# Optimization experiments

Hardware: AMD Instinct MI355X
Metric: run time of the kernel (lower is better)

The kernel has to match this reference:

```python
import jax, jax.numpy as jnp
import numpy as np

B, N, S, D1, D2 = 16, 4096, 1024, 128, 256
MLP = [256, 128]
BN_EPS = 1e-5


def setup_inputs() -> dict:
    key = jax.random.key(0)
    ks = jax.random.split(key, 12)
    inp = {
        "xyz1": jax.random.normal(ks[0], (B, 3, N), dtype=jnp.float32),
        "xyz2": jax.random.normal(ks[1], (B, 3, S), dtype=jnp.float32),
        "points1": jax.random.normal(ks[2], (B, D1, N), dtype=jnp.float32),
        "points2": jax.random.normal(ks[3], (B, D2, S), dtype=jnp.float32),
    }
    in_ch = D1 + D2  # 384
    chans = [in_ch] + MLP
    ki = 4
    for li in range(len(MLP)):
        cin, cout = chans[li], chans[li + 1]
        inp[f"w{li+1}"] = jax.random.normal(ks[ki], (cout, cin), dtype=jnp.float32) * (1.0 / np.sqrt(cin)); ki += 1
        inp[f"b{li+1}"] = jnp.zeros((cout,), dtype=jnp.float32)
        inp[f"g{li+1}"] = jnp.ones((cout,), dtype=jnp.float32)
        inp[f"beta{li+1}"] = jnp.zeros((cout,), dtype=jnp.float32)
    return inp


def _batchnorm1d(x, gamma, beta):
    # x: [B, C, N]; training-mode batch stats over (B, N)
    mean = jnp.mean(x, axis=(0, 2), keepdims=True)
    var = jnp.var(x, axis=(0, 2), keepdims=True)
    xhat = (x - mean) * jax.lax.rsqrt(var + BN_EPS)
    return xhat * gamma[None, :, None] + beta[None, :, None]


def reference(xyz1, xyz2, points1, points2, w1, b1, g1, beta1, w2, b2, g2, beta2):
    x1 = jnp.transpose(xyz1, (0, 2, 1))   # [B, N, 3]
    x2 = jnp.transpose(xyz2, (0, 2, 1))   # [B, S, 3]
    p2 = jnp.transpose(points2, (0, 2, 1))  # [B, S, D2]

    # squared pairwise distances [B, N, S]
    dists = jnp.sum((x1[:, :, None, :] - x2[:, None, :, :]) ** 2, axis=-1)
    # 3 smallest distances (original sorts then slices top-3)
    neg_d3, idx = jax.lax.top_k(-dists, 3)  # [B, N, 3]
    d3 = -neg_d3
    dist_recip = 1.0 / (d3 + 1e-8)
    weight = dist_recip / jnp.sum(dist_recip, axis=2, keepdims=True)  # [B, N, 3]

    # gather neighbor features: [B, N, 3, D2]
    feats = p2[jnp.arange(p2.shape[0])[:, None, None], idx]
    interp = jnp.sum(feats * weight[..., None], axis=2)  # [B, N, D2]

    p1 = jnp.transpose(points1, (0, 2, 1))  # [B, N, D1]
    new_points = jnp.concatenate([p1, interp], axis=-1)  # [B, N, D1+D2]
    x = jnp.transpose(new_points, (0, 2, 1))  # [B, C, N]

    for w, b, g, bt in ((w1, b1, g1, beta1), (w2, b2, g2, beta2)):
        x = jnp.einsum("oc,bcn->bon", w, x) + b[None, :, None]
        x = _batchnorm1d(x, g, bt)
        x = jax.nn.relu(x)
    return x
```

## Files before the change

kernel.cpp:

```cpp
#include <hip/hip_runtime.h>

typedef unsigned short u16;
typedef unsigned int   u32;
typedef __attribute__((ext_vector_type(8))) short bf16x8;
typedef __attribute__((ext_vector_type(4))) float f32x4;

#define NB   16
#define NPTS 4096
#define SPTS 1024
#define BNT  65536

__device__ __forceinline__ float bf2f(u16 u){ return __uint_as_float(((u32)u)<<16); }
__device__ __forceinline__ u16 f2bf(float f){
  u32 u = __float_as_uint(f);
  return (u16)((u + 0x7FFFu + ((u>>16)&1u))>>16);
}

__global__ __launch_bounds__(256) void convw_k(const float* __restrict__ w1, const float* __restrict__ w2,
                                               u16* __restrict__ w1b, u16* __restrict__ w2b){
  int i = blockIdx.x*256 + threadIdx.x;
  if (i < 98304) w1b[i] = f2bf(w1[i]);
  else { int j = i - 98304; w2b[j] = f2bf(w2[j]); }
}

__global__ __launch_bounds__(256) void transpose_k(const float* __restrict__ in, u16* __restrict__ out,
                                                   int C, int S, int ostride){
  __shared__ float tl[64][65];
  int t = threadIdx.x;
  int b = blockIdx.y;
  int s0 = blockIdx.x * 64;
  for (int ct = 0; ct < C; ct += 64){
    __syncthreads();
    for (int i = t; i < 4096; i += 256){
      int sl = i & 63, cl = i >> 6;
      tl[sl][cl] = in[((size_t)b*C + ct + cl)*S + s0 + sl];
    }
    __syncthreads();
    for (int i = t; i < 4096; i += 256){
      int cl = i & 63, sl = i >> 6;
      out[((size_t)b*S + s0 + sl)*ostride + ct + cl] = f2bf(tl[sl][cl]);
    }
  }
}

__global__ __launch_bounds__(512) void knn_k(const float* __restrict__ xyz1, const float* __restrict__ xyz2,
                                             const u16* __restrict__ p2t, u16* __restrict__ X){
  __shared__ float4 sxyz[SPTS];
  __shared__ float  pd[8][3][64];
  __shared__ int    pi[8][3][64];
  __shared__ float  swts[3][64];
  __shared__ int    sidx[3][64];
  int t  = threadIdx.x;
  int b  = blockIdx.x >> 6;
  int n0 = (blockIdx.x & 63) << 6;
  const float* x2b = xyz2 + (size_t)b*3*SPTS;
  for (int s = t; s < SPTS; s += 512)
    sxyz[s] = make_float4(x2b[s], x2b[SPTS+s], x2b[2*SPTS+s], 0.f);
  int q = t & 63, g = t >> 6;
  const float* x1b = xyz1 + (size_t)b*3*NPTS;
  int n = n0 + q;
  float qx = x1b[n], qy = x1b[NPTS+n], qz = x1b[2*NPTS+n];
  __syncthreads();

  float d0=3.4e38f, d1=3.4e38f, d2=3.4e38f;
  int   i0=0, i1=0, i2=0;
  int sBeg = g << 7, sEnd = sBeg + 128;
  for (int s = sBeg; s < sEnd; ++s){
    float4 p = sxyz[s];
    float dist;
    {
      #pragma clang fp contract(off)
      float dx = qx - p.x, dy = qy - p.y, dz = qz - p.z;
      dist = ((dx*dx) + (dy*dy)) + (dz*dz);
    }
    if (dist < d2){
      bool c1 = dist < d1, c0 = dist < d0;
      d2 = c1 ? d1 : dist;                 i2 = c1 ? i1 : s;
      float nd1 = c1 ? (c0 ? d0 : dist) : d1;
      int   ni1 = c1 ? (c0 ? i0 : s)    : i1;
      d0 = c0 ? dist : d0;                 i0 = c0 ? s : i0;
      d1 = nd1;                            i1 = ni1;
    }
  }
  pd[g][0][q]=d0; pd[g][1][q]=d1; pd[g][2][q]=d2;
  pi[g][0][q]=i0; pi[g][1][q]=i1; pi[g][2][q]=i2;
  __syncthreads();

  if (t < 64){
    float m0=3.4e38f, m1=3.4e38f, m2=3.4e38f;
    int   j0=0, j1=0, j2=0;
    #pragma unroll
    for (int gg = 0; gg < 8; ++gg){
      #pragma unroll
      for (int p = 0; p < 3; ++p){
        float dist = pd[gg][p][t]; int s = pi[gg][p][t];
        if (dist < m2){
          bool c1 = dist < m1, c0 = dist < m0;
          m2 = c1 ? m1 : dist;                 j2 = c1 ? j1 : s;
          float nd1 = c1 ? (c0 ? m0 : dist) : m1;
          int   ni1 = c1 ? (c0 ? j0 : s)    : j1;
          m0 = c0 ? dist : m0;                 j0 = c0 ? s : j0;
          m1 = nd1;                            j1 = ni1;
        }
      }
    }
    float r0 = 1.f/(m0 + 1e-8f), r1 = 1.f/(m1 + 1e-8f), r2 = 1.f/(m2 + 1e-8f);
    float rs = (r0 + r1) + r2;
    swts[0][t] = r0/rs; swts[1][t] = r1/rs; swts[2][t] = r2/rs;
    sidx[0][t] = j0;    sidx[1][t] = j1;    sidx[2][t] = j2;
  }
  __syncthreads();

  int w = t >> 6, lane = t & 63;
  for (int qq = w*8; qq < w*8 + 8; ++qq){
    float wa = swts[0][qq], wb = swts[1][qq], wc = swts[2][qq];
    int   j0 = sidx[0][qq], j1 = sidx[1][qq], j2 = sidx[2][qq];
    const ushort4 u0 = *(const ushort4*)(p2t + (((size_t)b*SPTS + j0)<<8) + (lane<<2));
    const ushort4 u1 = *(const ushort4*)(p2t + (((size_t)b*SPTS + j1)<<8) + (lane<<2));
    const ushort4 u2 = *(const ushort4*)(p2t + (((size_t)b*SPTS + j2)<<8) + (lane<<2));
    ushort4 ov;
    ov.x = f2bf(wa*bf2f(u0.x) + wb*bf2f(u1.x) + wc*bf2f(u2.x));
    ov.y = f2bf(wa*bf2f(u0.y) + wb*bf2f(u1.y) + wc*bf2f(u2.y));
    ov.z = f2bf(wa*bf2f(u0.z) + wb*bf2f(u1.z) + wc*bf2f(u2.z));
    ov.w = f2bf(wa*bf2f(u0.w) + wb*bf2f(u1.w) + wc*bf2f(u2.w));
    *(ushort4*)(X + ((size_t)b*NPTS + n0 + qq)*384 + 128 + (lane<<2)) = ov;
  }
}

__global__ __launch_bounds__(256) void gemm_k(const u16* __restrict__ A, const u16* __restrict__ Bw,
                                              u16* __restrict__ Cc, int K, int Nn,
                                              float* __restrict__ gsum, float* __restrict__ gsq){
  __shared__ u16 lA[128*32];
  __shared__ u16 lB[128*32];
  __shared__ float sums[128];
  __shared__ float sqs[128];
  int t = threadIdx.x, lane = t & 63, wid = t >> 6;
  int rowBase = blockIdx.x << 7, colBase = blockIdx.y << 7;
  int wm = wid >> 1, wn = wid & 1;
  int rr = lane >> 2, cb = (lane & 3) << 4;

  const char* pA0 = (const char*)A  + (((size_t)(rowBase + wid*32 + rr) * K) << 1) + cb;
  const char* pA1 = pA0 + (((size_t)16 * K) << 1);
  const char* pB0 = (const char*)Bw + (((size_t)(colBase + wid*32 + rr) * K) << 1) + cb;
  const char* pB1 = pB0 + (((size_t)16 * K) << 1);
  char* dA0 = (char*)lA + wid*2048; char* dA1 = dA0 + 1024;
  char* dB0 = (char*)lB + wid*2048; char* dB1 = dB0 + 1024;

  f32x4 z = {0.f, 0.f, 0.f, 0.f};
  f32x4 acc[4][4];
  #pragma unroll
  for (int m = 0; m < 4; ++m)
    #pragma unroll
    for (int n = 0; n < 4; ++n) acc[m][n] = z;

  for (int kk = 0; kk < K; kk += 32){
    size_t ko = ((size_t)kk) << 1;
    __builtin_amdgcn_global_load_lds((const __attribute__((address_space(1))) void*)(pA0 + ko),
                                     (__attribute__((address_space(3))) void*)dA0, 16, 0, 0);
    __builtin_amdgcn_global_load_lds((const __attribute__((address_space(1))) void*)(pA1 + ko),
                                     (__attribute__((address_space(3))) void*)dA1, 16, 0, 0);
    __builtin_amdgcn_global_load_lds((const __attribute__((address_space(1))) void*)(pB0 + ko),
                                     (__attribute__((address_space(3))) void*)dB0, 16, 0, 0);
    __builtin_amdgcn_global_load_lds((const __attribute__((address_space(1))) void*)(pB1 + ko),
                                     (__attribute__((address_space(3))) void*)dB1, 16, 0, 0);
    __syncthreads();
    bf16x8 af[4], bfr[4];
    #pragma unroll
    for (int m = 0; m < 4; ++m)
      af[m] = *(const bf16x8*)(lA + ((wm*64 + m*16 + (lane & 15)) << 5) + ((lane >> 4) << 3));
    #pragma unroll
    for (int n = 0; n < 4; ++n)
      bfr[n] = *(const bf16x8*)(lB + ((wn*64 + n*16 + (lane & 15)) << 5) + ((lane >> 4) << 3));
    #pragma unroll
    for (int m = 0; m < 4; ++m)
      #pragma unroll
      for (int n = 0; n < 4; ++n)
        acc[m][n] = __builtin_amdgcn_mfma_f32_16x16x32_bf16(af[m], bfr[n], acc[m][n], 0, 0, 0);
    __syncthreads();
  }

  if (t < 128){ sums[t] = 0.f; sqs[t] = 0.f; }
  __syncthreads();
  size_t rb = (size_t)rowBase + wm*64 + ((lane >> 4) << 2);
  int cbase = colBase + wn*64 + (lane & 15);
  #pragma unroll
  for (int n = 0; n < 4; ++n){
    float s = 0.f, q = 0.f;
    #pragma unroll
    for (int m = 0; m < 4; ++m){
      #pragma unroll
      for (int r = 0; r < 4; ++r){
        float v = acc[m][n][r];
        Cc[(rb + m*16 + r)*(size_t)Nn + cbase + n*16] = f2bf(v);
        s += v; q += v*v;
      }
    }
    int cl = wn*64 + n*16 + (lane & 15);
    atomicAdd(&sums[cl], s); atomicAdd(&sqs[cl], q);
  }
  __syncthreads();
  if (t < 128){
    atomicAdd(&gsum[colBase + t], sums[t]);
    atomicAdd(&gsq [colBase + t], sqs[t]);
  }
}

__global__ void finalize_k(const float* __restrict__ sum, const float* __restrict__ sq,
                           const float* __restrict__ g, const float* __restrict__ bet,
                           float* __restrict__ sc, float* __restrict__ sh, int C){
  int t = threadIdx.x;
  if (t < C){
    const float inv = 1.f/65536.f;
    float mean = sum[t]*inv;
    float var  = sq[t]*inv - mean*mean;
    float rstd = rsqrtf(var + 1e-5f);
    float s = g[t]*rstd;
    sc[t] = s;
    sh[t] = bet[t] - mean*s;
  }
}

__global__ __launch_bounds__(256) void bnrelu_k(const u16* __restrict__ y, u16* __restrict__ o,
                                                const float* __restrict__ sc, const float* __restrict__ sh){
  size_t i = ((size_t)blockIdx.x*256 + threadIdx.x)*8;
  ushort4 a = *(const ushort4*)(y + i);
  ushort4 b = *(const ushort4*)(y + i + 4);
  int c0 = (int)(i & 255);
  ushort4 oa, ob;
  float v;
  v = bf2f(a.x)*sc[c0+0] + sh[c0+0]; oa.x = f2bf(fmaxf(v, 0.f));
  v = bf2f(a.y)*sc[c0+1] + sh[c0+1]; oa.y = f2bf(fmaxf(v, 0.f));
  v = bf2f(a.z)*sc[c0+2] + sh[c0+2]; oa.z = f2bf(fmaxf(v, 0.f));
  v = bf2f(a.w)*sc[c0+3] + sh[c0+3]; oa.w = f2bf(fmaxf(v, 0.f));
  v = bf2f(b.x)*sc[c0+4] + sh[c0+4]; ob.x = f2bf(fmaxf(v, 0.f));
  v = bf2f(b.y)*sc[c0+5] + sh[c0+5]; ob.y = f2bf(fmaxf(v, 0.f));
  v = bf2f(b.z)*sc[c0+6] + sh[c0+6]; ob.z = f2bf(fmaxf(v, 0.f));
  v = bf2f(b.w)*sc[c0+7] + sh[c0+7]; ob.w = f2bf(fmaxf(v, 0.f));
  *(ushort4*)(o + i)     = oa;
  *(ushort4*)(o + i + 4) = ob;
}

__global__ __launch_bounds__(256) void finalout_k(const u16* __restrict__ y2, const float* __restrict__ sc,
                                                  const float* __restrict__ sh, float* __restrict__ out){
  __shared__ float tl[128][65];
  int t  = threadIdx.x;
  int b  = blockIdx.x >> 6;
  int n0 = (blockIdx.x & 63) << 6;
  for (int i = t; i < 8192; i += 256){
    int r = i >> 7, c = i & 127;
    float v = bf2f(y2[((size_t)b*NPTS + n0 + r)*128 + c]);
    v = fmaxf(v*sc[c] + sh[c], 0.f);
    tl[c][r] = v;
  }
  __syncthreads();
  for (int i = t; i < 8192; i += 256){
    int o = i >> 6, j = i & 63;
    out[(size_t)b*128*NPTS + (size_t)o*NPTS + n0 + j] = tl[o][j];
  }
}

extern "C" void kernel_launch(void* const* d_in, const int* in_sizes, int n_in,
                              void* d_out, int out_size, void* d_ws, size_t ws_size,
                              hipStream_t stream) {
  const float* xyz1    = (const float*)d_in[0];
  const float* xyz2    = (const float*)d_in[1];
  const float* points1 = (const float*)d_in[2];
  const float* points2 = (const float*)d_in[3];
  const float* w1      = (const float*)d_in[4];
  const float* g1      = (const float*)d_in[6];
  const float* beta1   = (const float*)d_in[7];
  const float* w2      = (const float*)d_in[8];
  const float* g2      = (const float*)d_in[10];
  const float* beta2   = (const float*)d_in[11];

  char* ws = (char*)d_ws;
  u16*  X    = (u16*)ws;
  u16*  Y1n  = (u16*)ws;
  u16*  Y2   = (u16*)(ws + 33554432);
  u16*  p2t  = (u16*)(ws + 50331648);
  u16*  Y1   = (u16*)(ws + 58720256);
  u16*  w1b  = (u16*)(ws + 92274688);
  u16*  w2b  = (u16*)(ws + 92471296);
  float* st  = (float*)(ws + 92536832);
  float* sum1 = st;        float* sq1 = st + 256;
  float* sum2 = st + 512;  float* sq2 = st + 640;
  float* sc1  = st + 768;  float* sh1 = st + 1024;
  float* sc2  = st + 1280; float* sh2 = st + 1408;

  hipMemsetAsync(st, 0, 768*sizeof(float), stream);

  convw_k<<<512, 256, 0, stream>>>(w1, w2, w1b, w2b);
  transpose_k<<<dim3(64, 16), 256, 0, stream>>>(points1, X,   128, NPTS, 384);
  transpose_k<<<dim3(16, 16), 256, 0, stream>>>(points2, p2t, 256, SPTS, 256);
  knn_k<<<1024, 512, 0, stream>>>(xyz1, xyz2, p2t, X);
  gemm_k<<<dim3(512, 2), 256, 0, stream>>>(X, w1b, Y1, 384, 256, sum1, sq1);
  finalize_k<<<1, 256, 0, stream>>>(sum1, sq1, g1, beta1, sc1, sh1, 256);
  bnrelu_k<<<8192, 256, 0, stream>>>(Y1, Y1n, sc1, sh1);
  gemm_k<<<dim3(512, 1), 256, 0, stream>>>(Y1n, w2b, Y2, 256, 128, sum2, sq2);
  finalize_k<<<1, 256, 0, stream>>>(sum2, sq2, g2, beta2, sc2, sh2, 128);
  finalout_k<<<1024, 256, 0, stream>>>(Y2, sc2, sh2, (float*)d_out);
}
```

Before: 168.1 us.

## Fuse BN1+ReLU into second GEMM, swizzled 64x128 tiles, partial-sum BN stats

Removes the standalone BN+ReLU pass by applying scale/shift/ReLU while staging the second GEMM's A operand into LDS. The two GEMMs are rewritten with 64x128 tiles, K-step 64 and an XOR-swizzled LDS layout to reduce bank conflicts. BN statistics use per-block partial sums reduced by a multi-block finalize kernel instead of global atomics and a memset. The second GEMM's A path now goes through registers rather than direct global-to-LDS loads, which may add latency.

```diff
diff --git a/kernel.cpp b/kernel.cpp
--- a/kernel.cpp
+++ b/kernel.cpp
@@ -3,6 +3,7 @@
 typedef unsigned short u16;
 typedef unsigned int   u32;
 typedef __attribute__((ext_vector_type(8))) short bf16x8;
+typedef __attribute__((ext_vector_type(8))) unsigned short u16x8;
 typedef __attribute__((ext_vector_type(4))) float f32x4;
 
 #define NB   16
@@ -127,117 +128,252 @@
   }
 }
 
-__global__ __launch_bounds__(256) void gemm_k(const u16* __restrict__ A, const u16* __restrict__ Bw,
-                                              u16* __restrict__ Cc, int K, int Nn,
-                                              float* __restrict__ gsum, float* __restrict__ gsq){
-  __shared__ u16 lA[128*32];
-  __shared__ u16 lB[128*32];
-  __shared__ float sums[128];
-  __shared__ float sqs[128];
+
+__global__ __launch_bounds__(256) void gemm1_k(const u16* __restrict__ A, const u16* __restrict__ Bw,
+                                               u16* __restrict__ Cc,
+                                               float* __restrict__ psum, float* __restrict__ psq){
+  const int K = 384, Nn = 256;
+  __shared__ u16 lA[64*64];
+  __shared__ u16 lB[128*64];
+  __shared__ float sums[128], sqs[128];
   int t = threadIdx.x, lane = t & 63, wid = t >> 6;
-  int rowBase = blockIdx.x << 7, colBase = blockIdx.y << 7;
+  int rowBase = blockIdx.x << 6, colBase = blockIdx.y << 7;
   int wm = wid >> 1, wn = wid & 1;
-  int rr = lane >> 2, cb = (lane & 3) << 4;
-
-  const char* pA0 = (const char*)A  + (((size_t)(rowBase + wid*32 + rr) * K) << 1) + cb;
-  const char* pA1 = pA0 + (((size_t)16 * K) << 1);
-  const char* pB0 = (const char*)Bw + (((size_t)(colBase + wid*32 + rr) * K) << 1) + cb;
-  const char* pB1 = pB0 + (((size_t)16 * K) << 1);
-  char* dA0 = (char*)lA + wid*2048; char* dA1 = dA0 + 1024;
-  char* dB0 = (char*)lB + wid*2048; char* dB1 = dB0 + 1024;
-
-  f32x4 z = {0.f, 0.f, 0.f, 0.f};
-  f32x4 acc[4][4];
-  #pragma unroll
-  for (int m = 0; m < 4; ++m)
+
+  const char* pA[2]; char* dA[2];
+  #pragma unroll
+  for (int j = 0; j < 2; ++j){
+    int L = j*4096 + wid*1024 + lane*16;
+    int row = L >> 7, kb = L & 127;
+    int kbs = kb ^ ((row & 7) << 4);
+    pA[j] = (const char*)A + ((size_t)(rowBase + row)*K)*2 + kbs;
+    dA[j] = (char*)lA + j*4096 + wid*1024;
+  }
+  const char* pB[4]; char* dB[4];
+  #pragma unroll
+  for (int j = 0; j < 4; ++j){
+    int L = j*4096 + wid*1024 + lane*16;
+    int row = L >> 7, kb = L & 127;
+    int kbs = kb ^ ((row & 7) << 4);
+    pB[j] = (const char*)Bw + ((size_t)(colBase + row)*K)*2 + kbs;
+    dB[j] = (char*)lB + j*4096 + wid*1024;
+  }
+
+  f32x4 z = {0.f,0.f,0.f,0.f};
+  f32x4 acc[2][4];
+  #pragma unroll
+  for (int m = 0; m < 2; ++m)
     #pragma unroll
     for (int n = 0; n < 4; ++n) acc[m][n] = z;
 
-  for (int kk = 0; kk < K; kk += 32){
-    size_t ko = ((size_t)kk) << 1;
-    __builtin_amdgcn_global_load_lds((const __attribute__((address_space(1))) void*)(pA0 + ko),
-                                     (__attribute__((address_space(3))) void*)dA0, 16, 0, 0);
-    __builtin_amdgcn_global_load_lds((const __attribute__((address_space(1))) void*)(pA1 + ko),
-                                     (__attribute__((address_space(3))) void*)dA1, 16, 0, 0);
-    __builtin_amdgcn_global_load_lds((const __attribute__((address_space(1))) void*)(pB0 + ko),
-                                     (__attribute__((address_space(3))) void*)dB0, 16, 0, 0);
-    __builtin_amdgcn_global_load_lds((const __attribute__((address_space(1))) void*)(pB1 + ko),
-                                     (__attribute__((address_space(3))) void*)dB1, 16, 0, 0);
-    __syncthreads();
-    bf16x8 af[4], bfr[4];
-    #pragma unroll
-    for (int m = 0; m < 4; ++m)
-      af[m] = *(const bf16x8*)(lA + ((wm*64 + m*16 + (lane & 15)) << 5) + ((lane >> 4) << 3));
-    #pragma unroll
-    for (int n = 0; n < 4; ++n)
-      bfr[n] = *(const bf16x8*)(lB + ((wn*64 + n*16 + (lane & 15)) << 5) + ((lane >> 4) << 3));
-    #pragma unroll
-    for (int m = 0; m < 4; ++m)
-      #pragma unroll
-      for (int n = 0; n < 4; ++n)
-        acc[m][n] = __builtin_amdgcn_mfma_f32_16x16x32_bf16(af[m], bfr[n], acc[m][n], 0, 0, 0);
+  for (int kk = 0; kk < K; kk += 64){
+    size_t ko = (size_t)kk * 2;
+    #pragma unroll
+    for (int j = 0; j < 2; ++j)
+      __builtin_amdgcn_global_load_lds((const __attribute__((address_space(1))) void*)(pA[j] + ko),
+                                       (__attribute__((address_space(3))) void*)dA[j], 16, 0, 0);
+    #pragma unroll
+    for (int j = 0; j < 4; ++j)
+      __builtin_amdgcn_global_load_lds((const __attribute__((address_space(1))) void*)(pB[j] + ko),
+                                       (__attribute__((address_space(3))) void*)dB[j], 16, 0, 0);
+    __syncthreads();
+    bf16x8 af[2][2], bfv[4][2];
+    #pragma unroll
+    for (int m = 0; m < 2; ++m){
+      int row = wm*32 + m*16 + (lane & 15);
+      int sw = (row & 7) << 4;
+      #pragma unroll
+      for (int ks = 0; ks < 2; ++ks){
+        int kb = (ks*64 + ((lane >> 4) << 4)) ^ sw;
+        af[m][ks] = *(const bf16x8*)((const char*)lA + row*128 + kb);
+      }
+    }
+    #pragma unroll
+    for (int n = 0; n < 4; ++n){
+      int row = wn*64 + n*16 + (lane & 15);
+      int sw = (row & 7) << 4;
+      #pragma unroll
+      for (int ks = 0; ks < 2; ++ks){
+        int kb = (ks*64 + ((lane >> 4) << 4)) ^ sw;
+        bfv[n][ks] = *(const bf16x8*)((const char*)lB + row*128 + kb);
+      }
+    }
+    #pragma unroll
+    for (int ks = 0; ks < 2; ++ks)
+      #pragma unroll
+      for (int m = 0; m < 2; ++m)
+        #pragma unroll
+        for (int n = 0; n < 4; ++n)
+          acc[m][n] = __builtin_amdgcn_mfma_f32_16x16x32_bf16(af[m][ks], bfv[n][ks], acc[m][n], 0, 0, 0);
     __syncthreads();
   }
 
   if (t < 128){ sums[t] = 0.f; sqs[t] = 0.f; }
   __syncthreads();
-  size_t rb = (size_t)rowBase + wm*64 + ((lane >> 4) << 2);
-  int cbase = colBase + wn*64 + (lane & 15);
+  int colb = colBase + wn*64 + (lane & 15);
+  int rowb = rowBase + wm*32 + ((lane >> 4) << 2);
   #pragma unroll
   for (int n = 0; n < 4; ++n){
-    float s = 0.f, q = 0.f;
-    #pragma unroll
-    for (int m = 0; m < 4; ++m){
+    float s = 0.f, qq2 = 0.f;
+    #pragma unroll
+    for (int m = 0; m < 2; ++m){
       #pragma unroll
       for (int r = 0; r < 4; ++r){
         float v = acc[m][n][r];
-        Cc[(rb + m*16 + r)*(size_t)Nn + cbase + n*16] = f2bf(v);
-        s += v; q += v*v;
-      }
-    }
-    int cl = wn*64 + n*16 + (lane & 15);
-    atomicAdd(&sums[cl], s); atomicAdd(&sqs[cl], q);
+        Cc[(size_t)(rowb + m*16 + r)*Nn + colb + n*16] = f2bf(v);
+        s += v; qq2 += v*v;
+      }
+    }
+    atomicAdd(&sums[wn*64 + n*16 + (lane & 15)], s);
+    atomicAdd(&sqs [wn*64 + n*16 + (lane & 15)], qq2);
   }
   __syncthreads();
   if (t < 128){
-    atomicAdd(&gsum[colBase + t], sums[t]);
-    atomicAdd(&gsq [colBase + t], sqs[t]);
-  }
-}
-
-__global__ void finalize_k(const float* __restrict__ sum, const float* __restrict__ sq,
-                           const float* __restrict__ g, const float* __restrict__ bet,
-                           float* __restrict__ sc, float* __restrict__ sh, int C){
-  int t = threadIdx.x;
-  if (t < C){
+    int c = colBase + t;
+    psum[(size_t)c*1024 + blockIdx.x] = sums[t];
+    psq [(size_t)c*1024 + blockIdx.x] = sqs[t];
+  }
+}
+
+__global__ __launch_bounds__(256) void gemm2_k(const u16* __restrict__ A, const u16* __restrict__ Bw,
+                                               u16* __restrict__ Cc,
+                                               const float* __restrict__ sc, const float* __restrict__ sh,
+                                               float* __restrict__ psum, float* __restrict__ psq){
+  const int K = 256, Nn = 128;
+  __shared__ u16 lA[64*64];
+  __shared__ u16 lB[128*64];
+  __shared__ float sums[128], sqs[128];
+  int t = threadIdx.x, lane = t & 63, wid = t >> 6;
+  int rowBase = blockIdx.x << 6;
+  int wm = wid >> 1, wn = wid & 1;
+
+  const char* pB[4]; char* dB[4];
+  #pragma unroll
+  for (int j = 0; j < 4; ++j){
+    int L = j*4096 + wid*1024 + lane*16;
+    int row = L >> 7, kb = L & 127;
+    int kbs = kb ^ ((row & 7) << 4);
+    pB[j] = (const char*)Bw + ((size_t)row*K)*2 + kbs;
+    dB[j] = (char*)lB + j*4096 + wid*1024;
+  }
+  int arow = t & 63, achunk = t >> 6;
+  const u16* pArow = A + (size_t)(rowBase + arow)*K + achunk*16;
+  int asw = (arow & 7) << 4;
+  char* wA0 = (char*)lA + arow*128 + (((achunk*32)      ) ^ asw);
+  char* wA1 = (char*)lA + arow*128 + (((achunk*32) + 16 ) ^ asw);
+
+  f32x4 z = {0.f,0.f,0.f,0.f};
+  f32x4 acc[2][4];
+  #pragma unroll
+  for (int m = 0; m < 2; ++m)
+    #pragma unroll
+    for (int n = 0; n < 4; ++n) acc[m][n] = z;
+
+  for (int kk = 0; kk < K; kk += 64){
+    size_t ko = (size_t)kk * 2;
+    #pragma unroll
+    for (int j = 0; j < 4; ++j)
+      __builtin_amdgcn_global_load_lds((const __attribute__((address_space(1))) void*)(pB[j] + ko),
+                                       (__attribute__((address_space(3))) void*)dB[j], 16, 0, 0);
+    u16x8 y0 = *(const u16x8*)(pArow + kk);
+    u16x8 y1 = *(const u16x8*)(pArow + kk + 8);
+    int k0 = kk + achunk*16;
+    bf16x8 o0, o1;
+    #pragma unroll
+    for (int j = 0; j < 8; ++j){
+      float v = bf2f((u16)y0[j]) * sc[k0 + j] + sh[k0 + j];
+      o0[j] = (short)f2bf(fmaxf(v, 0.f));
+    }
+    #pragma unroll
+    for (int j = 0; j < 8; ++j){
+      float v = bf2f((u16)y1[j]) * sc[k0 + 8 + j] + sh[k0 + 8 + j];
+      o1[j] = (short)f2bf(fmaxf(v, 0.f));
+    }
+    *(bf16x8*)wA0 = o0;
+    *(bf16x8*)wA1 = o1;
+    __syncthreads();
+    bf16x8 af[2][2], bfv[4][2];
+    #pragma unroll
+    for (int m = 0; m < 2; ++m){
+      int row = wm*32 + m*16 + (lane & 15);
+      int sw = (row & 7) << 4;
+      #pragma unroll
+      for (int ks = 0; ks < 2; ++ks){
+        int kb = (ks*64 + ((lane >> 4) << 4)) ^ sw;
+        af[m][ks] = *(const bf16x8*)((const char*)lA + row*128 + kb);
+      }
+    }
+    #pragma unroll
+    for (int n = 0; n < 4; ++n){
+      int row = wn*64 + n*16 + (lane & 15);
+      int sw = (row & 7) << 4;
+      #pragma unroll
+      for (int ks = 0; ks < 2; ++ks){
+        int kb = (ks*64 + ((lane >> 4) << 4)) ^ sw;
+        bfv[n][ks] = *(const bf16x8*)((const char*)lB + row*128 + kb);
+      }
+    }
+    #pragma unroll
+    for (int ks = 0; ks < 2; ++ks)
+      #pragma unroll
+      for (int m = 0; m < 2; ++m)
+        #pragma unroll
+        for (int n = 0; n < 4; ++n)
+          acc[m][n] = __builtin_amdgcn_mfma_f32_16x16x32_bf16(af[m][ks], bfv[n][ks], acc[m][n], 0, 0, 0);
+    __syncthreads();
+  }
+
+  if (t < 128){ sums[t] = 0.f; sqs[t] = 0.f; }
+  __syncthreads();
+  int colb = wn*64 + (lane & 15);
+  int rowb = rowBase + wm*32 + ((lane >> 4) << 2);
+  #pragma unroll
+  for (int n = 0; n < 4; ++n){
+    float s = 0.f, qq2 = 0.f;
+    #pragma unroll
+    for (int m = 0; m < 2; ++m){
+      #pragma unroll
+      for (int r = 0; r < 4; ++r){
+        float v = acc[m][n][r];
+        Cc[(size_t)(rowb + m*16 + r)*Nn + colb + n*16] = f2bf(v);
+        s += v; qq2 += v*v;
+      }
+    }
+    atomicAdd(&sums[colb + n*16], s);
+    atomicAdd(&sqs [colb + n*16], qq2);
+  }
+  __syncthreads();
+  if (t < 128){
+    psum[(size_t)t*1024 + blockIdx.x] = sums[t];
+    psq [(size_t)t*1024 + blockIdx.x] = sqs[t];
+  }
+}
+
+__global__ __launch_bounds__(256) void finalize2_k(const float* __restrict__ psum, const float* __restrict__ psq,
+                                                   const float* __restrict__ g, const float* __restrict__ bet,
+                                                   float* __restrict__ sc, float* __restrict__ sh){
+  __shared__ float rs[256], rq[256];
+  int c = blockIdx.x, t = threadIdx.x;
+  float s = 0.f, q = 0.f;
+  for (int rt = t; rt < 1024; rt += 256){
+    s += psum[(size_t)c*1024 + rt];
+    q += psq [(size_t)c*1024 + rt];
+  }
+  rs[t] = s; rq[t] = q;
+  __syncthreads();
+  for (int off = 128; off; off >>= 1){
+    if (t < off){ rs[t] += rs[t+off]; rq[t] += rq[t+off]; }
+    __syncthreads();
+  }
+  if (t == 0){
     const float inv = 1.f/65536.f;
-    float mean = sum[t]*inv;
-    float var  = sq[t]*inv - mean*mean;
+    float mean = rs[0]*inv;
+    float var  = rq[0]*inv - mean*mean;
     float rstd = rsqrtf(var + 1e-5f);
-    float s = g[t]*rstd;
-    sc[t] = s;
-    sh[t] = bet[t] - mean*s;
-  }
-}
-
-__global__ __launch_bounds__(256) void bnrelu_k(const u16* __restrict__ y, u16* __restrict__ o,
-                                                const float* __restrict__ sc, const float* __restrict__ sh){
-  size_t i = ((size_t)blockIdx.x*256 + threadIdx.x)*8;
-  ushort4 a = *(const ushort4*)(y + i);
-  ushort4 b = *(const ushort4*)(y + i + 4);
-  int c0 = (int)(i & 255);
-  ushort4 oa, ob;
-  float v;
-  v = bf2f(a.x)*sc[c0+0] + sh[c0+0]; oa.x = f2bf(fmaxf(v, 0.f));
-  v = bf2f(a.y)*sc[c0+1] + sh[c0+1]; oa.y = f2bf(fmaxf(v, 0.f));
-  v = bf2f(a.z)*sc[c0+2] + sh[c0+2]; oa.z = f2bf(fmaxf(v, 0.f));
-  v = bf2f(a.w)*sc[c0+3] + sh[c0+3]; oa.w = f2bf(fmaxf(v, 0.f));
-  v = bf2f(b.x)*sc[c0+4] + sh[c0+4]; ob.x = f2bf(fmaxf(v, 0.f));
-  v = bf2f(b.y)*sc[c0+5] + sh[c0+5]; ob.y = f2bf(fmaxf(v, 0.f));
-  v = bf2f(b.z)*sc[c0+6] + sh[c0+6]; ob.z = f2bf(fmaxf(v, 0.f));
-  v = bf2f(b.w)*sc[c0+7] + sh[c0+7]; ob.w = f2bf(fmaxf(v, 0.f));
-  *(ushort4*)(o + i)     = oa;
-  *(ushort4*)(o + i + 4) = ob;
+    float scl  = g[c]*rstd;
+    sc[c] = scl;
+    sh[c] = bet[c] - mean*scl;
+  }
 }
 
 __global__ __launch_bounds__(256) void finalout_k(const u16* __restrict__ y2, const float* __restrict__ sc,
@@ -275,28 +411,27 @@
 
   char* ws = (char*)d_ws;
   u16*  X    = (u16*)ws;
-  u16*  Y1n  = (u16*)ws;
-  u16*  Y2   = (u16*)(ws + 33554432);
-  u16*  p2t  = (u16*)(ws + 50331648);
-  u16*  Y1   = (u16*)(ws + 58720256);
+  u16*  Y2   = (u16*)ws;
+  u16*  Y1   = (u16*)(ws + 50331648);
+  u16*  p2t  = (u16*)(ws + 83886080);
   u16*  w1b  = (u16*)(ws + 92274688);
   u16*  w2b  = (u16*)(ws + 92471296);
-  float* st  = (float*)(ws + 92536832);
-  float* sum1 = st;        float* sq1 = st + 256;
-  float* sum2 = st + 512;  float* sq2 = st + 640;
-  float* sc1  = st + 768;  float* sh1 = st + 1024;
-  float* sc2  = st + 1280; float* sh2 = st + 1408;
-
-  hipMemsetAsync(st, 0, 768*sizeof(float), stream);
+  float* psum1 = (float*)(ws + 83886080);
+  float* psq1  = (float*)(ws + 84934656);
+  float* psum2 = (float*)(ws + 85983232);
+  float* psq2  = (float*)(ws + 86507520);
+  float* sc1   = (float*)(ws + 87031808);
+  float* sh1   = (float*)(ws + 87032832);
+  float* sc2   = (float*)(ws + 87033856);
+  float* sh2   = (float*)(ws + 87034368);
 
   convw_k<<<512, 256, 0, stream>>>(w1, w2, w1b, w2b);
   transpose_k<<<dim3(64, 16), 256, 0, stream>>>(points1, X,   128, NPTS, 384);
   transpose_k<<<dim3(16, 16), 256, 0, stream>>>(points2, p2t, 256, SPTS, 256);
   knn_k<<<1024, 512, 0, stream>>>(xyz1, xyz2, p2t, X);
-  gemm_k<<<dim3(512, 2), 256, 0, stream>>>(X, w1b, Y1, 384, 256, sum1, sq1);
-  finalize_k<<<1, 256, 0, stream>>>(sum1, sq1, g1, beta1, sc1, sh1, 256);
-  bnrelu_k<<<8192, 256, 0, stream>>>(Y1, Y1n, sc1, sh1);
-  gemm_k<<<dim3(512, 1), 256, 0, stream>>>(Y1n, w2b, Y2, 256, 128, sum2, sq2);
-  finalize_k<<<1, 256, 0, stream>>>(sum2, sq2, g2, beta2, sc2, sh2, 128);
+  gemm1_k<<<dim3(1024, 2), 256, 0, stream>>>(X, w1b, Y1, psum1, psq1);
+  finalize2_k<<<256, 256, 0, stream>>>(psum1, psq1, g1, beta1, sc1, sh1);
+  gemm2_k<<<1024, 256, 0, stream>>>(Y1, w2b, Y2, sc1, sh1, psum2, psq2);
+  finalize2_k<<<128, 256, 0, stream>>>(psum2, psq2, g2, beta2, sc2, sh2);
   finalout_k<<<1024, 256, 0, stream>>>(Y2, sc2, sh2, (float*)d_out);
 }
```

Result: faster. 154.9 us (-7.9%).
